# Performance work log

Hardware: AMD Instinct MI355X
Metric: run time of the kernel (lower is better)

The kernel has to match this reference:

```python
import jax, jax.numpy as jnp
import numpy as np

AT_ID = 5       # tokenizer id of '@'
CITSEG_ID = 7   # tokenizer id of 'CITSEG'


def setup_inputs() -> dict:
    key = jax.random.key(0)
    ks = jax.random.split(key, 12)
    B, S, H = 256, 512, 768
    CIT, D, NC = 750, 1518, 6
    s = lambda n: 1.0 / np.sqrt(n)
    return {
        "tokens": jax.random.randint(ks[0], (B, S), 0, 100),
        "hidden_states": jax.random.normal(ks[1], (B, S, H), jnp.float32),
        "proj_w": jax.random.normal(ks[2], (H, CIT), jnp.float32) * s(H),
        "proj_b": jax.random.normal(ks[3], (CIT,), jnp.float32) * 0.02,
        "enc_w": jax.random.normal(ks[4], (CIT, CIT), jnp.float32) * s(CIT),
        "enc_b": jax.random.normal(ks[5], (CIT,), jnp.float32) * 0.02,
        "w1": jax.random.normal(ks[6], (D, 2 * D), jnp.float32) * s(D),
        "b1": jax.random.normal(ks[7], (2 * D,), jnp.float32) * 0.02,
        "w2": jax.random.normal(ks[8], (2 * D, 2 * D), jnp.float32) * s(2 * D),
        "b2": jax.random.normal(ks[9], (2 * D,), jnp.float32) * 0.02,
        "w3": jax.random.normal(ks[10], (2 * D, NC), jnp.float32) * s(2 * D),
        "b3": jax.random.normal(ks[11], (NC,), jnp.float32) * 0.02,
    }


def _forward(tokens, hidden_states, proj_w, proj_b, enc_w, enc_b,
             w1, b1, w2, b2, w3, b3):
    B, S, H = hidden_states.shape
    idx = jnp.arange(S)[None, :]                       # [1,S]
    BIG = S + 1

    # --- ctx_pooler: masked max over tokens outside the [start,end] '@' span ---
    at_mask = tokens == AT_ID                          # [B,S]
    first = jnp.min(jnp.where(at_mask, idx, BIG), axis=1)            # [B]
    second = jnp.min(jnp.where(at_mask & (idx > first[:, None]), idx, BIG), axis=1)
    ge2 = at_mask.sum(axis=1) >= 2
    start = jnp.where(ge2, first, 0)
    end = jnp.where(ge2, second, S)                    # end=S excludes everything
    keep = (idx < start[:, None]) | (idx > end[:, None])             # [B,S]
    neg = jnp.finfo(hidden_states.dtype).min
    pooled = jnp.max(jnp.where(keep[:, :, None], hidden_states, neg), axis=1)  # [B,H]
    pooled = jnp.where(keep.any(axis=1)[:, None], pooled, 0.0)

    # --- CITSEG token gather + projection (zero row if absent) ---
    c_mask = tokens == CITSEG_ID
    c_first = jnp.min(jnp.where(c_mask, idx, BIG), axis=1)           # [B]
    has_c = c_mask.any(axis=1)
    safe_pos = jnp.minimum(c_first, S - 1)
    cit_h = jnp.take_along_axis(hidden_states, safe_pos[:, None, None], axis=1)[:, 0]  # [B,H]
    cit = (cit_h @ proj_w + proj_b) * has_c[:, None].astype(hidden_states.dtype)       # [B,750]

    # --- citseg_encoder (modeled as Linear 750->750) ---
    cit_enc = cit @ enc_w + enc_b

    # --- MLP head ---
    x = jnp.concatenate([pooled, cit_enc], axis=1)     # [B,1518]
    x = jax.nn.relu(x @ w1 + b1)
    x = jax.nn.relu(x @ w2 + b2)
    return x @ w3 + b3                                 # [B,num_class]


def reference(tokens, hidden_states, proj_w, proj_b, enc_w, enc_b,
              w1, b1, w2, b2, w3, b3):
    return _forward(tokens, hidden_states, proj_w, proj_b, enc_w, enc_b,
                    w1, b1, w2, b2, w3, b3)
```

## Files before the change

### kernel.cpp

```cpp
#include <hip/hip_runtime.h>
#include <hip/hip_bf16.h>

typedef __attribute__((ext_vector_type(8))) short bf16x8;
typedef __attribute__((ext_vector_type(4))) float f32x4;
typedef __attribute__((ext_vector_type(4))) unsigned short u16x4;

#define NEGINF (-3.4028234663852886e38f)

__device__ __forceinline__ unsigned short f2b(float f) {
    union { float f; unsigned u; } x; x.f = f;
    unsigned r = x.u + 0x7FFFu + ((x.u >> 16) & 1u);
    return (unsigned short)(r >> 16);
}
__device__ __forceinline__ float b2f(unsigned short b) {
    union { unsigned u; float f; } x; x.u = ((unsigned)b) << 16;
    return x.f;
}

__global__ __launch_bounds__(64) void scan_k(const int* __restrict__ tokens,
                                             int* __restrict__ meta) {
    const int S = 512, BIG = 1 << 20;
    int b = blockIdx.x, l = threadIdx.x;
    const int* row = tokens + (size_t)b * S;
    int base = l * 8;
    int toks[8];
#pragma unroll
    for (int i = 0; i < 8; ++i) toks[i] = row[base + i];
    int am = 0, cnt = 0, minAt = BIG, minC = BIG;
#pragma unroll
    for (int i = 0; i < 8; ++i) {
        if (toks[i] == 5) { am |= 1 << i; cnt++; if (base + i < minAt) minAt = base + i; }
        if (toks[i] == 7) { if (base + i < minC) minC = base + i; }
    }
    for (int off = 1; off < 64; off <<= 1) {
        minAt = min(minAt, __shfl_xor(minAt, off));
        minC  = min(minC,  __shfl_xor(minC,  off));
        cnt  += __shfl_xor(cnt, off);
    }
    int first = minAt;
    int minAt2 = BIG;
#pragma unroll
    for (int i = 0; i < 8; ++i)
        if ((am >> i) & 1) { int idx = base + i; if (idx > first && idx < minAt2) minAt2 = idx; }
    for (int off = 1; off < 64; off <<= 1) minAt2 = min(minAt2, __shfl_xor(minAt2, off));
    if (l == 0) {
        int ge2 = (cnt >= 2) ? 1 : 0;
        int start = ge2 ? first : 0;
        int end = ge2 ? minAt2 : S;
        int anyKeep = (ge2 && (start > 0 || end < S - 1)) ? 1 : 0;
        int has_c = (minC < S) ? 1 : 0;
        int cpos = min(minC, S - 1);
        int* m = meta + b * 6;
        m[0] = start; m[1] = end; m[2] = cpos; m[3] = has_c; m[4] = anyKeep; m[5] = 0;
    }
}

__global__ __launch_bounds__(192) void pool_k(const float* __restrict__ hs,
                                              const int* __restrict__ meta,
                                              float* __restrict__ part) {
    int b = blockIdx.x >> 3, ch = blockIdx.x & 7;
    int start = meta[b * 6 + 0], end = meta[b * 6 + 1];
    int t = threadIdx.x;
    f32x4 m = { NEGINF, NEGINF, NEGINF, NEGINF };
    const float* basep = hs + (size_t)b * 512 * 768 + t * 4;
    int s0 = ch * 64;
#pragma unroll 4
    for (int s = s0; s < s0 + 64; ++s) {
        if (s >= start && s <= end) continue;
        f32x4 v = *(const f32x4*)(basep + (size_t)s * 768);
#pragma unroll
        for (int j = 0; j < 4; ++j) m[j] = fmaxf(m[j], v[j]);
    }
    *(f32x4*)(part + ((size_t)b * 8 + ch) * 768 + t * 4) = m;
}

__global__ __launch_bounds__(192) void pack_k(const float* __restrict__ hs,
                                              const float* __restrict__ part,
                                              const int* __restrict__ meta,
                                              unsigned short* __restrict__ xA,
                                              unsigned short* __restrict__ citA) {
    int b = blockIdx.x, t = threadIdx.x;
    const float* p = part + (size_t)b * 8 * 768 + t * 4;
    f32x4 m = *(const f32x4*)p;
#pragma unroll
    for (int ch = 1; ch < 8; ++ch) {
        f32x4 v = *(const f32x4*)(p + (size_t)ch * 768);
#pragma unroll
        for (int j = 0; j < 4; ++j) m[j] = fmaxf(m[j], v[j]);
    }
    if (!meta[b * 6 + 4]) {
        f32x4 z = {0.f, 0.f, 0.f, 0.f};
        m = z;
    }
    u16x4 o;
#pragma unroll
    for (int j = 0; j < 4; ++j) o[j] = f2b(m[j]);
    *(u16x4*)(xA + (size_t)b * 1536 + t * 4) = o;

    int cpos = meta[b * 6 + 2];
    f32x4 c = *(const f32x4*)(hs + ((size_t)b * 512 + cpos) * 768 + t * 4);
    u16x4 co;
#pragma unroll
    for (int j = 0; j < 4; ++j) co[j] = f2b(c[j]);
    *(u16x4*)(citA + (size_t)b * 768 + t * 4) = co;
}

__global__ __launch_bounds__(256) void trans_k(const float* __restrict__ in, int K, int N,
                                               unsigned short* __restrict__ out, int ldo) {
    __shared__ float tile[32][33];
    int n0 = blockIdx.x * 32, k0 = blockIdx.y * 32;
    int tx = threadIdx.x, ty = threadIdx.y;
#pragma unroll
    for (int i = 0; i < 4; ++i) {
        int k = k0 + ty * 4 + i, n = n0 + tx;
        tile[ty * 4 + i][tx] = (k < K && n < N) ? in[(size_t)k * N + n] : 0.f;
    }
    __syncthreads();
#pragma unroll
    for (int i = 0; i < 4; ++i) {
        int n = n0 + ty * 4 + i, k = k0 + tx;
        out[(size_t)n * ldo + k] = f2b(tile[tx][ty * 4 + i]);
    }
}

template<int EPI>
__global__ __launch_bounds__(256) void gemm_k(
    const unsigned short* __restrict__ A, int lda,
    const unsigned short* __restrict__ Bt, int ldb,
    const float* __restrict__ bias, const int* __restrict__ meta,
    unsigned short* __restrict__ X, int ldx, int Nreal, int Kp) {
    __shared__ unsigned short As[64 * 64];
    __shared__ unsigned short Bs[64 * 64];
    const int tid = threadIdx.x;
    const int wid = tid >> 6, lane = tid & 63;
    const int m0 = blockIdx.y * 64, n0 = blockIdx.x * 64;
    const int wr = wid >> 1, wc = wid & 1;
    f32x4 acc[2][2];
    const f32x4 zero = {0.f, 0.f, 0.f, 0.f};
#pragma unroll
    for (int mi = 0; mi < 2; ++mi)
#pragma unroll
        for (int nj = 0; nj < 2; ++nj) acc[mi][nj] = zero;

    const int rl = lane >> 3;
    const int c8 = lane & 7;

    for (int kt = 0; kt < Kp; kt += 64) {
        bf16x8 va[2], vb[2];
#pragma unroll
        for (int p = 0; p < 2; ++p) {
            int row = p * 32 + wid * 8 + rl;
            va[p] = *(const bf16x8*)(A + (size_t)(m0 + row) * lda + kt + c8 * 8);
            vb[p] = *(const bf16x8*)(Bt + (size_t)(n0 + row) * ldb + kt + c8 * 8);
        }
        __syncthreads();
#pragma unroll
        for (int p = 0; p < 2; ++p) {
            int row = p * 32 + wid * 8 + rl;
            int dst = row * 64 + ((c8 ^ (row & 7)) * 8);
            *(bf16x8*)(As + dst) = va[p];
            *(bf16x8*)(Bs + dst) = vb[p];
        }
        __syncthreads();
#pragma unroll
        for (int kk = 0; kk < 2; ++kk) {
            int k8 = kk * 4 + (lane >> 4);
            bf16x8 af[2], bfr[2];
#pragma unroll
            for (int mi = 0; mi < 2; ++mi) {
                int row = wr * 32 + mi * 16 + (lane & 15);
                af[mi] = *(const bf16x8*)(As + row * 64 + ((k8 ^ (row & 7)) * 8));
            }
#pragma unroll
            for (int nj = 0; nj < 2; ++nj) {
                int row = wc * 32 + nj * 16 + (lane & 15);
                bfr[nj] = *(const bf16x8*)(Bs + row * 64 + ((k8 ^ (row & 7)) * 8));
            }
#pragma unroll
            for (int mi = 0; mi < 2; ++mi)
#pragma unroll
                for (int nj = 0; nj < 2; ++nj)
                    acc[mi][nj] = __builtin_amdgcn_mfma_f32_16x16x32_bf16(
                        af[mi], bfr[nj], acc[mi][nj], 0, 0, 0);
        }
    }
#pragma unroll
    for (int mi = 0; mi < 2; ++mi) {
        int rowb = m0 + wr * 32 + mi * 16 + (lane >> 4) * 4;
#pragma unroll
        for (int nj = 0; nj < 2; ++nj) {
            int col = n0 + wc * 32 + nj * 16 + (lane & 15);
            float bv = (col < Nreal) ? bias[col] : 0.f;
#pragma unroll
            for (int i = 0; i < 4; ++i) {
                int row = rowb + i;
                float v = acc[mi][nj][i] + bv;
                if (EPI == 0) v *= (meta[row * 6 + 3] ? 1.f : 0.f);
                if (EPI == 2) v = fmaxf(v, 0.f);
                if (col >= Nreal) v = 0.f;
                X[(size_t)row * ldx + col] = f2b(v);
            }
        }
    }
}

__global__ __launch_bounds__(384) void out_k(const unsigned short* __restrict__ x2,
                                             const unsigned short* __restrict__ w3T,
                                             const float* __restrict__ b3,
                                             float* __restrict__ out) {
    int b = blockIdx.x;
    int wid = threadIdx.x >> 6, lane = threadIdx.x & 63;
    const unsigned short* xr = x2 + (size_t)b * 3072;
    const unsigned short* wr = w3T + (size_t)wid * 3072;
    float s = 0.f;
    for (int k0 = lane * 8; k0 < 3072; k0 += 512) {
        bf16x8 xv = *(const bf16x8*)(xr + k0);
        bf16x8 wv = *(const bf16x8*)(wr + k0);
#pragma unroll
        for (int j = 0; j < 8; ++j)
            s += b2f((unsigned short)xv[j]) * b2f((unsigned short)wv[j]);
    }
    for (int off = 1; off < 64; off <<= 1) s += __shfl_xor(s, off);
    if (lane == 0) out[b * 6 + wid] = s + b3[wid];
}

extern "C" void kernel_launch(void* const* d_in, const int* in_sizes, int n_in,
                              void* d_out, int out_size, void* d_ws, size_t ws_size,
                              hipStream_t stream) {
    const int*   tokens = (const int*)d_in[0];
    const float* hs     = (const float*)d_in[1];
    const float* proj_w = (const float*)d_in[2];
    const float* proj_b = (const float*)d_in[3];
    const float* enc_w  = (const float*)d_in[4];
    const float* enc_b  = (const float*)d_in[5];
    const float* w1 = (const float*)d_in[6];
    const float* b1 = (const float*)d_in[7];
    const float* w2 = (const float*)d_in[8];
    const float* b2 = (const float*)d_in[9];
    const float* w3 = (const float*)d_in[10];
    const float* b3 = (const float*)d_in[11];
    float* out = (float*)d_out;

    char* ws = (char*)d_ws;
    size_t off = 0;
    auto alloc = [&](size_t bytes) {
        void* p = ws + off;
        off = (off + bytes + 255) & ~(size_t)255;
        return p;
    };
    int* meta            = (int*)alloc(256 * 6 * sizeof(int));
    float* part          = (float*)alloc((size_t)256 * 8 * 768 * sizeof(float));
    unsigned short* xA   = (unsigned short*)alloc((size_t)256 * 1536 * 2);
    unsigned short* citA = (unsigned short*)alloc((size_t)256 * 768 * 2);
    unsigned short* citB = (unsigned short*)alloc((size_t)256 * 768 * 2);
    unsigned short* x1   = (unsigned short*)alloc((size_t)256 * 3072 * 2);
    unsigned short* x2   = (unsigned short*)alloc((size_t)256 * 3072 * 2);
    unsigned short* projT= (unsigned short*)alloc((size_t)768 * 768 * 2);
    unsigned short* encT = (unsigned short*)alloc((size_t)768 * 768 * 2);
    unsigned short* w1T  = (unsigned short*)alloc((size_t)3072 * 1536 * 2);
    unsigned short* w2T  = (unsigned short*)alloc((size_t)3072 * 3072 * 2);
    unsigned short* w3T  = (unsigned short*)alloc((size_t)32 * 3072 * 2);

    scan_k<<<256, 64, 0, stream>>>(tokens, meta);
    pool_k<<<2048, 192, 0, stream>>>(hs, meta, part);
    pack_k<<<256, 192, 0, stream>>>(hs, part, meta, xA, citA);

    trans_k<<<dim3(24, 24), dim3(32, 8), 0, stream>>>(proj_w, 768, 750, projT, 768);
    trans_k<<<dim3(24, 24), dim3(32, 8), 0, stream>>>(enc_w, 750, 750, encT, 768);
    trans_k<<<dim3(96, 48), dim3(32, 8), 0, stream>>>(w1, 1518, 3036, w1T, 1536);
    trans_k<<<dim3(96, 96), dim3(32, 8), 0, stream>>>(w2, 3036, 3036, w2T, 3072);
    trans_k<<<dim3(1, 96),  dim3(32, 8), 0, stream>>>(w3, 3036, 6, w3T, 3072);

    gemm_k<0><<<dim3(12, 4), 256, 0, stream>>>(citA, 768, projT, 768, proj_b, meta,
                                               citB, 768, 750, 768);
    gemm_k<1><<<dim3(12, 4), 256, 0, stream>>>(citB, 768, encT, 768, enc_b, meta,
                                               xA + 768, 1536, 750, 768);
    gemm_k<2><<<dim3(48, 4), 256, 0, stream>>>(xA, 1536, w1T, 1536, b1, meta,
                                               x1, 3072, 3036, 1536);
    gemm_k<2><<<dim3(48, 4), 256, 0, stream>>>(x1, 3072, w2T, 3072, b2, meta,
                                               x2, 3072, 3036, 3072);
    out_k<<<256, 384, 0, stream>>>(x2, w3T, b3, out);
}
```

Baseline: 184.9 us.

## Merge prep kernels, double-buffer GEMM via direct-to-LDS loads, split pool loop

The token scan and the four weight transposes are merged into one launch, which removes several small kernel launches. The GEMM now uses 128-wide K tiles, double-buffered in LDS and filled with global_load_lds, so global loads for the next tile overlap MFMA work on the current one. The pooling loop is split into two ranges around the excluded span instead of branching on every row. The output layer reads fp32 w3 directly, which drops the w3 transpose; the cost is uncoalesced strided reads of w3 and more LDS per GEMM block.

```diff
diff --git a/kernel.cpp b/kernel.cpp
--- a/kernel.cpp
+++ b/kernel.cpp
@@ -17,41 +17,79 @@
     return x.f;
 }
 
-__global__ __launch_bounds__(64) void scan_k(const int* __restrict__ tokens,
-                                             int* __restrict__ meta) {
-    const int S = 512, BIG = 1 << 20;
-    int b = blockIdx.x, l = threadIdx.x;
-    const int* row = tokens + (size_t)b * S;
-    int base = l * 8;
-    int toks[8];
-#pragma unroll
-    for (int i = 0; i < 8; ++i) toks[i] = row[base + i];
-    int am = 0, cnt = 0, minAt = BIG, minC = BIG;
-#pragma unroll
-    for (int i = 0; i < 8; ++i) {
-        if (toks[i] == 5) { am |= 1 << i; cnt++; if (base + i < minAt) minAt = base + i; }
-        if (toks[i] == 7) { if (base + i < minC) minC = base + i; }
-    }
-    for (int off = 1; off < 64; off <<= 1) {
-        minAt = min(minAt, __shfl_xor(minAt, off));
-        minC  = min(minC,  __shfl_xor(minC,  off));
-        cnt  += __shfl_xor(cnt, off);
-    }
-    int first = minAt;
-    int minAt2 = BIG;
-#pragma unroll
-    for (int i = 0; i < 8; ++i)
-        if ((am >> i) & 1) { int idx = base + i; if (idx > first && idx < minAt2) minAt2 = idx; }
-    for (int off = 1; off < 64; off <<= 1) minAt2 = min(minAt2, __shfl_xor(minAt2, off));
-    if (l == 0) {
-        int ge2 = (cnt >= 2) ? 1 : 0;
-        int start = ge2 ? first : 0;
-        int end = ge2 ? minAt2 : S;
-        int anyKeep = (ge2 && (start > 0 || end < S - 1)) ? 1 : 0;
-        int has_c = (minC < S) ? 1 : 0;
-        int cpos = min(minC, S - 1);
-        int* m = meta + b * 6;
-        m[0] = start; m[1] = end; m[2] = cpos; m[3] = has_c; m[4] = anyKeep; m[5] = 0;
+__device__ __forceinline__ void load_lds16(const void* g, void* l) {
+    __builtin_amdgcn_global_load_lds((const __attribute__((address_space(1))) void*)g,
+                                     (__attribute__((address_space(3))) void*)l, 16, 0, 0);
+}
+
+__device__ __forceinline__ void trans_tile(const float* __restrict__ in, int K, int N,
+                                           unsigned short* __restrict__ out, int ldo,
+                                           int bx, int by, int tid, float (*tile)[33]) {
+    int n0 = bx * 32, k0 = by * 32;
+    int tx = tid & 31, ty = tid >> 5;
+#pragma unroll
+    for (int i = 0; i < 4; ++i) {
+        int k = k0 + ty * 4 + i, n = n0 + tx;
+        tile[ty * 4 + i][tx] = (k < K && n < N) ? in[(size_t)k * N + n] : 0.f;
+    }
+    __syncthreads();
+#pragma unroll
+    for (int i = 0; i < 4; ++i) {
+        int n = n0 + ty * 4 + i, k = k0 + tx;
+        out[(size_t)n * ldo + k] = f2b(tile[tx][ty * 4 + i]);
+    }
+}
+
+__global__ __launch_bounds__(256) void prep_k(
+    const int* __restrict__ tokens, int* __restrict__ meta,
+    const float* __restrict__ proj_w, const float* __restrict__ enc_w,
+    const float* __restrict__ w1, const float* __restrict__ w2,
+    unsigned short* __restrict__ projT, unsigned short* __restrict__ encT,
+    unsigned short* __restrict__ w1T, unsigned short* __restrict__ w2T) {
+    __shared__ float tile[32][33];
+    int bid = blockIdx.x, tid = threadIdx.x;
+    if (bid < 64) {
+        const int S = 512, BIG = 1 << 20;
+        int b = bid * 4 + (tid >> 6), l = tid & 63;
+        const int* row = tokens + (size_t)b * S;
+        int base = l * 8;
+        int toks[8];
+#pragma unroll
+        for (int i = 0; i < 8; ++i) toks[i] = row[base + i];
+        int am = 0, cnt = 0, minAt = BIG, minC = BIG;
+#pragma unroll
+        for (int i = 0; i < 8; ++i) {
+            if (toks[i] == 5) { am |= 1 << i; cnt++; if (base + i < minAt) minAt = base + i; }
+            if (toks[i] == 7) { if (base + i < minC) minC = base + i; }
+        }
+        for (int off = 1; off < 64; off <<= 1) {
+            minAt = min(minAt, __shfl_xor(minAt, off));
+            minC  = min(minC,  __shfl_xor(minC,  off));
+            cnt  += __shfl_xor(cnt, off);
+        }
+        int first = minAt, minAt2 = BIG;
+#pragma unroll
+        for (int i = 0; i < 8; ++i)
+            if ((am >> i) & 1) { int idx = base + i; if (idx > first && idx < minAt2) minAt2 = idx; }
+        for (int off = 1; off < 64; off <<= 1) minAt2 = min(minAt2, __shfl_xor(minAt2, off));
+        if (l == 0) {
+            int ge2 = (cnt >= 2) ? 1 : 0;
+            int start = ge2 ? first : 0;
+            int end = ge2 ? minAt2 : S;
+            int anyKeep = (ge2 && (start > 0 || end < S - 1)) ? 1 : 0;
+            int has_c = (minC < S) ? 1 : 0;
+            int cpos = min(minC, S - 1);
+            int* m = meta + b * 6;
+            m[0] = start; m[1] = end; m[2] = cpos; m[3] = has_c; m[4] = anyKeep; m[5] = 0;
+        }
+    } else if (bid < 640) {
+        int r = bid - 64;   trans_tile(proj_w, 768, 750, projT, 768, r % 24, r / 24, tid, tile);
+    } else if (bid < 1216) {
+        int r = bid - 640;  trans_tile(enc_w, 750, 750, encT, 768, r % 24, r / 24, tid, tile);
+    } else if (bid < 5824) {
+        int r = bid - 1216; trans_tile(w1, 1518, 3036, w1T, 1536, r % 96, r / 96, tid, tile);
+    } else {
+        int r = bid - 5824; trans_tile(w2, 3036, 3036, w2T, 3072, r % 96, r / 96, tid, tile);
     }
 }
 
@@ -63,10 +101,17 @@
     int t = threadIdx.x;
     f32x4 m = { NEGINF, NEGINF, NEGINF, NEGINF };
     const float* basep = hs + (size_t)b * 512 * 768 + t * 4;
-    int s0 = ch * 64;
+    int s0 = ch * 64, hi = s0 + 64;
+    int e1 = min(start, hi);
+    int s2 = max(end + 1, s0);
 #pragma unroll 4
-    for (int s = s0; s < s0 + 64; ++s) {
-        if (s >= start && s <= end) continue;
+    for (int s = s0; s < e1; ++s) {
+        f32x4 v = *(const f32x4*)(basep + (size_t)s * 768);
+#pragma unroll
+        for (int j = 0; j < 4; ++j) m[j] = fmaxf(m[j], v[j]);
+    }
+#pragma unroll 4
+    for (int s = s2; s < hi; ++s) {
         f32x4 v = *(const f32x4*)(basep + (size_t)s * 768);
 #pragma unroll
         for (int j = 0; j < 4; ++j) m[j] = fmaxf(m[j], v[j]);
@@ -105,36 +150,39 @@
     *(u16x4*)(citA + (size_t)b * 768 + t * 4) = co;
 }
 
-__global__ __launch_bounds__(256) void trans_k(const float* __restrict__ in, int K, int N,
-                                               unsigned short* __restrict__ out, int ldo) {
-    __shared__ float tile[32][33];
-    int n0 = blockIdx.x * 32, k0 = blockIdx.y * 32;
-    int tx = threadIdx.x, ty = threadIdx.y;
-#pragma unroll
-    for (int i = 0; i < 4; ++i) {
-        int k = k0 + ty * 4 + i, n = n0 + tx;
-        tile[ty * 4 + i][tx] = (k < K && n < N) ? in[(size_t)k * N + n] : 0.f;
-    }
-    __syncthreads();
-#pragma unroll
-    for (int i = 0; i < 4; ++i) {
-        int n = n0 + ty * 4 + i, k = k0 + tx;
-        out[(size_t)n * ldo + k] = f2b(tile[tx][ty * 4 + i]);
-    }
-}
-
 template<int EPI>
-__global__ __launch_bounds__(256) void gemm_k(
+__global__ __launch_bounds__(256, 2) void gemm_k(
     const unsigned short* __restrict__ A, int lda,
     const unsigned short* __restrict__ Bt, int ldb,
     const float* __restrict__ bias, const int* __restrict__ meta,
     unsigned short* __restrict__ X, int ldx, int Nreal, int Kp) {
-    __shared__ unsigned short As[64 * 64];
-    __shared__ unsigned short Bs[64 * 64];
+    __shared__ __align__(16) unsigned short As[2][64 * 128];
+    __shared__ __align__(16) unsigned short Bs[2][64 * 128];
     const int tid = threadIdx.x;
     const int wid = tid >> 6, lane = tid & 63;
     const int m0 = blockIdx.y * 64, n0 = blockIdx.x * 64;
     const int wr = wid >> 1, wc = wid & 1;
+    const int c_lin = lane & 15;
+    const int rsub = lane >> 4;
+
+    int aoff[4], boff[4], ldst[4];
+#pragma unroll
+    for (int i = 0; i < 4; ++i) {
+        int r = wid * 16 + i * 4 + rsub;
+        int csrc = (c_lin ^ (r & 15)) << 3;
+        aoff[i] = (m0 + r) * lda + csrc;
+        boff[i] = (n0 + r) * ldb + csrc;
+        ldst[i] = (wid * 16 + i * 4) * 128;
+    }
+    int cswz[4];
+#pragma unroll
+    for (int ks = 0; ks < 4; ++ks) cswz[ks] = ((ks * 4 + (lane >> 4)) ^ c_lin) << 3;
+    int arow[2], brow[2];
+#pragma unroll
+    for (int mi = 0; mi < 2; ++mi) arow[mi] = (wr * 32 + mi * 16 + c_lin) * 128;
+#pragma unroll
+    for (int nj = 0; nj < 2; ++nj) brow[nj] = (wc * 32 + nj * 16 + c_lin) * 128;
+
     f32x4 acc[2][2];
     const f32x4 zero = {0.f, 0.f, 0.f, 0.f};
 #pragma unroll
@@ -142,40 +190,28 @@
 #pragma unroll
         for (int nj = 0; nj < 2; ++nj) acc[mi][nj] = zero;
 
-    const int rl = lane >> 3;
-    const int c8 = lane & 7;
-
-    for (int kt = 0; kt < Kp; kt += 64) {
-        bf16x8 va[2], vb[2];
-#pragma unroll
-        for (int p = 0; p < 2; ++p) {
-            int row = p * 32 + wid * 8 + rl;
-            va[p] = *(const bf16x8*)(A + (size_t)(m0 + row) * lda + kt + c8 * 8);
-            vb[p] = *(const bf16x8*)(Bt + (size_t)(n0 + row) * ldb + kt + c8 * 8);
-        }
+    auto stage = [&](int nb, int kt) {
+#pragma unroll
+        for (int i = 0; i < 4; ++i) load_lds16(A + aoff[i] + kt, &As[nb][ldst[i]]);
+#pragma unroll
+        for (int i = 0; i < 4; ++i) load_lds16(Bt + boff[i] + kt, &Bs[nb][ldst[i]]);
+    };
+
+    const int nt = Kp >> 7;
+    stage(0, 0);
+    int cb = 0;
+    for (int t = 0; t < nt; ++t) {
         __syncthreads();
-#pragma unroll
-        for (int p = 0; p < 2; ++p) {
-            int row = p * 32 + wid * 8 + rl;
-            int dst = row * 64 + ((c8 ^ (row & 7)) * 8);
-            *(bf16x8*)(As + dst) = va[p];
-            *(bf16x8*)(Bs + dst) = vb[p];
-        }
-        __syncthreads();
-#pragma unroll
-        for (int kk = 0; kk < 2; ++kk) {
-            int k8 = kk * 4 + (lane >> 4);
+        if (t + 1 < nt) stage(cb ^ 1, (t + 1) << 7);
+        const unsigned short* as = As[cb];
+        const unsigned short* bs = Bs[cb];
+#pragma unroll
+        for (int ks = 0; ks < 4; ++ks) {
             bf16x8 af[2], bfr[2];
 #pragma unroll
-            for (int mi = 0; mi < 2; ++mi) {
-                int row = wr * 32 + mi * 16 + (lane & 15);
-                af[mi] = *(const bf16x8*)(As + row * 64 + ((k8 ^ (row & 7)) * 8));
-            }
-#pragma unroll
-            for (int nj = 0; nj < 2; ++nj) {
-                int row = wc * 32 + nj * 16 + (lane & 15);
-                bfr[nj] = *(const bf16x8*)(Bs + row * 64 + ((k8 ^ (row & 7)) * 8));
-            }
+            for (int mi = 0; mi < 2; ++mi) af[mi] = *(const bf16x8*)(as + arow[mi] + cswz[ks]);
+#pragma unroll
+            for (int nj = 0; nj < 2; ++nj) bfr[nj] = *(const bf16x8*)(bs + brow[nj] + cswz[ks]);
 #pragma unroll
             for (int mi = 0; mi < 2; ++mi)
 #pragma unroll
@@ -183,6 +219,7 @@
                     acc[mi][nj] = __builtin_amdgcn_mfma_f32_16x16x32_bf16(
                         af[mi], bfr[nj], acc[mi][nj], 0, 0, 0);
         }
+        cb ^= 1;
     }
 #pragma unroll
     for (int mi = 0; mi < 2; ++mi) {
@@ -204,24 +241,29 @@
     }
 }
 
-__global__ __launch_bounds__(384) void out_k(const unsigned short* __restrict__ x2,
-                                             const unsigned short* __restrict__ w3T,
+__global__ __launch_bounds__(256) void out_k(const unsigned short* __restrict__ x2,
+                                             const float* __restrict__ w3,
                                              const float* __restrict__ b3,
                                              float* __restrict__ out) {
-    int b = blockIdx.x;
-    int wid = threadIdx.x >> 6, lane = threadIdx.x & 63;
+    int b = blockIdx.x, t = threadIdx.x;
+    int wid = t >> 6, lane = t & 63;
+    float s[6] = {0.f, 0.f, 0.f, 0.f, 0.f, 0.f};
     const unsigned short* xr = x2 + (size_t)b * 3072;
-    const unsigned short* wr = w3T + (size_t)wid * 3072;
-    float s = 0.f;
-    for (int k0 = lane * 8; k0 < 3072; k0 += 512) {
-        bf16x8 xv = *(const bf16x8*)(xr + k0);
-        bf16x8 wv = *(const bf16x8*)(wr + k0);
-#pragma unroll
-        for (int j = 0; j < 8; ++j)
-            s += b2f((unsigned short)xv[j]) * b2f((unsigned short)wv[j]);
-    }
-    for (int off = 1; off < 64; off <<= 1) s += __shfl_xor(s, off);
-    if (lane == 0) out[b * 6 + wid] = s + b3[wid];
+    for (int k = t; k < 3036; k += 256) {
+        float x = b2f(xr[k]);
+#pragma unroll
+        for (int j = 0; j < 6; ++j) s[j] += x * w3[(size_t)k * 6 + j];
+    }
+#pragma unroll
+    for (int j = 0; j < 6; ++j)
+        for (int off = 1; off < 64; off <<= 1) s[j] += __shfl_xor(s[j], off);
+    __shared__ float red[4][6];
+    if (lane == 0) {
+#pragma unroll
+        for (int j = 0; j < 6; ++j) red[wid][j] = s[j];
+    }
+    __syncthreads();
+    if (t < 6) out[b * 6 + t] = red[0][t] + red[1][t] + red[2][t] + red[3][t] + b3[t];
 }
 
 extern "C" void kernel_launch(void* const* d_in, const int* in_sizes, int n_in,
@@ -259,17 +301,11 @@
     unsigned short* encT = (unsigned short*)alloc((size_t)768 * 768 * 2);
     unsigned short* w1T  = (unsigned short*)alloc((size_t)3072 * 1536 * 2);
     unsigned short* w2T  = (unsigned short*)alloc((size_t)3072 * 3072 * 2);
-    unsigned short* w3T  = (unsigned short*)alloc((size_t)32 * 3072 * 2);
-
-    scan_k<<<256, 64, 0, stream>>>(tokens, meta);
+
+    prep_k<<<15040, 256, 0, stream>>>(tokens, meta, proj_w, enc_w, w1, w2,
+                                      projT, encT, w1T, w2T);
     pool_k<<<2048, 192, 0, stream>>>(hs, meta, part);
     pack_k<<<256, 192, 0, stream>>>(hs, part, meta, xA, citA);
-
-    trans_k<<<dim3(24, 24), dim3(32, 8), 0, stream>>>(proj_w, 768, 750, projT, 768);
-    trans_k<<<dim3(24, 24), dim3(32, 8), 0, stream>>>(enc_w, 750, 750, encT, 768);
-    trans_k<<<dim3(96, 48), dim3(32, 8), 0, stream>>>(w1, 1518, 3036, w1T, 1536);
-    trans_k<<<dim3(96, 96), dim3(32, 8), 0, stream>>>(w2, 3036, 3036, w2T, 3072);
-    trans_k<<<dim3(1, 96),  dim3(32, 8), 0, stream>>>(w3, 3036, 6, w3T, 3072);
 
     gemm_k<0><<<dim3(12, 4), 256, 0, stream>>>(citA, 768, projT, 768, proj_b, meta,
                                                citB, 768, 750, 768);
@@ -279,5 +315,5 @@
                                                x1, 3072, 3036, 1536);
     gemm_k<2><<<dim3(48, 4), 256, 0, stream>>>(x1, 3072, w2T, 3072, b2, meta,
                                                x2, 3072, 3036, 3072);
-    out_k<<<256, 384, 0, stream>>>(x2, w3T, b3, out);
-}
+    out_k<<<256, 256, 0, stream>>>(x2, w3, b3, out);
+}
```

New measurement: 165.5 us. 1.12x faster.
